# Performance work log

Hardware: AMD Instinct MI355X
Metric: run time of the kernel (lower is better)

## Reference

```python
import jax, jax.numpy as jnp
import numpy as np

V, E, H = 32000, 256, 512   # vocab, embed_dim, hidden_dim
B, S, T = 16, 512, 128      # batch, src_len, tgt_len
PAD = 0
H2 = 2 * H                  # decoder hidden size


def setup_inputs() -> dict:
    key = jax.random.key(0)
    ks = jax.random.split(key, 20)
    g = lambda k, shape: jax.random.normal(k, shape, dtype=jnp.float32) * 0.05
    emb = g(ks[0], (V, E)).at[PAD].set(0.0)  # padding_idx row zeroed
    inp = {
        "src": jax.random.randint(ks[18], (B, S), 0, V, dtype=jnp.int32),
        "tgt": jax.random.randint(ks[19], (B, T), 0, V, dtype=jnp.int32),
        "emb": emb,
        # encoder forward direction (torch gate order i,f,g,o)
        "Wih_f": g(ks[1], (4 * H, E)), "Whh_f": g(ks[2], (4 * H, H)),
        "bih_f": g(ks[3], (4 * H,)),   "bhh_f": g(ks[4], (4 * H,)),
        # encoder backward direction
        "Wih_b": g(ks[5], (4 * H, E)), "Whh_b": g(ks[6], (4 * H, H)),
        "bih_b": g(ks[7], (4 * H,)),   "bhh_b": g(ks[8], (4 * H,)),
        # decoder LSTM: input E+2H, hidden 2H
        "Wih_d": g(ks[9], (4 * H2, E + H2)), "Whh_d": g(ks[10], (4 * H2, H2)),
        "bih_d": g(ks[11], (4 * H2,)),       "bhh_d": g(ks[12], (4 * H2,)),
        # attention Linear(4H -> 2H)
        "Wa": g(ks[13], (H2, 2 * H2)), "ba": g(ks[14], (H2,)),
        # output Linear(2H -> V)
        "Wo": g(ks[15], (V, H2)), "bo": g(ks[16], (V,)),
    }
    return inp


def _lstm_cell(x, h, c, Wih, Whh, bih, bhh):
    z = x @ Wih.T + h @ Whh.T + bih + bhh
    i, f, g, o = jnp.split(z, 4, axis=-1)
    c = jax.nn.sigmoid(f) * c + jax.nn.sigmoid(i) * jnp.tanh(g)
    h = jax.nn.sigmoid(o) * jnp.tanh(c)
    return h, c


def _lstm_scan(xs, h0, c0, Wih, Whh, bih, bhh):
    def step(carry, x):
        h, c = _lstm_cell(x, carry[0], carry[1], Wih, Whh, bih, bhh)
        return (h, c), h
    (hT, cT), hs = jax.lax.scan(step, (h0, c0), xs)
    return hs, hT, cT


def reference(src, tgt, emb, Wih_f, Whh_f, bih_f, bhh_f, Wih_b, Whh_b, bih_b, bhh_b,
              Wih_d, Whh_d, bih_d, bhh_d, Wa, ba, Wo, bo):
    z = jnp.zeros((B, H), dtype=emb.dtype)
    xs = emb[src].transpose(1, 0, 2)                       # [S,B,E]
    hs_f, hTf, _ = _lstm_scan(xs,        z, z, Wih_f, Whh_f, bih_f, bhh_f)
    hs_b, hTb, _ = _lstm_scan(xs[::-1],  z, z, Wih_b, Whh_b, bih_b, bhh_b)
    enc_out = jnp.concatenate([hs_f, hs_b[::-1]], -1).transpose(1, 0, 2)  # [B,S,2H]
    h = jnp.concatenate([hTf, hTb], -1)                    # decoder h0 [B,2H]
    c = jnp.zeros_like(h)  # note: original reuses encoder c_n; see combined c0 below
    # original uses c_n (last cells) as decoder c0:
    _, _, cTf = _lstm_scan(xs, z, z, Wih_f, Whh_f, bih_f, bhh_f)[1], None, None
    # recompute cleanly (scan already returned cT above; redo properly):
    hs_f2, hTf2, cTf2 = _lstm_scan(xs,       z, z, Wih_f, Whh_f, bih_f, bhh_f)
    hs_b2, hTb2, cTb2 = _lstm_scan(xs[::-1], z, z, Wih_b, Whh_b, bih_b, bhh_b)
    c = jnp.concatenate([cTf2, cTb2], -1)

    Wa_h, Wa_e = Wa[:, :H2], Wa[:, H2:]
    enc_proj = jnp.einsum('bsd,kd->bsk', enc_out, Wa_e) + ba  # [B,S,2H]

    dec_xs = emb[tgt[:, :T - 1]].transpose(1, 0, 2)        # [T-1,B,E] teacher-forced

    def dec_step(carry, x):
        h, c = carry
        energy = jnp.tanh(enc_proj + (h @ Wa_h.T)[:, None, :])  # [B,S,2H]
        w = jax.nn.softmax(energy.sum(-1), axis=1)              # [B,S]
        ctx = jnp.einsum('bs,bsd->bd', w, enc_out)              # [B,2H]
        xi = jnp.concatenate([x, ctx], -1)                      # [B,E+2H]
        h, c = _lstm_cell(xi, h, c, Wih_d, Whh_d, bih_d, bhh_d)
        pred = h @ Wo.T + bo                                    # [B,V]
        return (h, c), pred

    _, preds = jax.lax.scan(dec_step, (h, c), dec_xs)           # [T-1,B,V]
    outputs = jnp.concatenate(
        [jnp.zeros((B, 1, V), dtype=preds.dtype), preds.transpose(1, 0, 2)], axis=1)
    return outputs
```

## Files before the change

kernel.cpp:

```cpp
#include <hip/hip_runtime.h>

typedef unsigned int uint;
typedef unsigned short ushort;
typedef unsigned long long ull;
typedef __attribute__((ext_vector_type(8))) short bf16x8;
typedef __attribute__((ext_vector_type(4))) float f32x4;

static constexpr int V_ = 32000, E_ = 256, H_ = 512, B_ = 16, S_ = 512, T_ = 128;
static constexpr int H2_ = 1024, G4_ = 2048, D4_ = 4096, KXI_ = 2304;
static constexpr int DSTEPS = T_ - 1;
static constexpr int MD = 2048;
static constexpr int NWG_DEC = 256;
static constexpr float LOG2E = 1.4426950408889634f;
static constexpr int ASTR = 2312;

#define DEVFN __device__ __forceinline__

DEVFN ushort f2bf(float f){ uint u = __builtin_bit_cast(uint, f); u += 0x7fffu + ((u>>16)&1u); return (ushort)(u>>16); }
DEVFN float bf2f(ushort h){ uint u = ((uint)h)<<16; return __builtin_bit_cast(float, u); }
DEVFN float fsig(float x){ float e = __builtin_amdgcn_exp2f(-LOG2E*x); return __builtin_amdgcn_rcpf(1.f+e); }
DEVFN float ftanh(float x){ x = fminf(15.f,fmaxf(-15.f,x)); float e = __builtin_amdgcn_exp2f(2.f*LOG2E*x); return (e-1.f)*__builtin_amdgcn_rcpf(e+1.f); }
DEVFN f32x4 mfma16(bf16x8 a, bf16x8 b, f32x4 c){ return __builtin_amdgcn_mfma_f32_16x16x32_bf16(a,b,c,0,0,0); }

struct ull2v{ ull x, y; };
DEVFN ull ald64(const void* p){ return __hip_atomic_load((const ull*)p, __ATOMIC_RELAXED, __HIP_MEMORY_SCOPE_AGENT); }
DEVFN uint ald32u(const uint* p){ return __hip_atomic_load(p, __ATOMIC_RELAXED, __HIP_MEMORY_SCOPE_AGENT); }
DEVFN float ald_f32(const float* p){ uint v = __hip_atomic_load((const uint*)p, __ATOMIC_RELAXED, __HIP_MEMORY_SCOPE_AGENT); return __builtin_bit_cast(float, v); }
DEVFN void ast32(float* p, float v){ __hip_atomic_store(p, v, __ATOMIC_RELAXED, __HIP_MEMORY_SCOPE_AGENT); }
DEVFN void ast16(ushort* p, ushort v){ __hip_atomic_store(p, v, __ATOMIC_RELAXED, __HIP_MEMORY_SCOPE_AGENT); }
DEVFN void astu(uint* p, uint v){ __hip_atomic_store(p, v, __ATOMIC_RELAXED, __HIP_MEMORY_SCOPE_AGENT); }

DEVFN void lbar(uint* lflags, int grp, int mem, int tid, uint& rnd){
  __syncthreads();
  rnd++;
  if (tid==0) astu(lflags + grp*16 + mem, rnd);
  if (tid<16){
    while (ald32u(lflags + grp*16 + tid) < rnd) __builtin_amdgcn_s_sleep(1);
  }
  __syncthreads();
}

__global__ void k_init(uint* __restrict__ flags, uint* __restrict__ hgf, uint* __restrict__ hgb,
                       uint* __restrict__ hU, uint* __restrict__ ctxU){
  int i = blockIdx.x*256 + threadIdx.x;
  if (i < 1024) flags[i] = 0;
  if (i < 2*B_*H_){ hgf[i]=0u; hgb[i]=0u; }
  if (i < B_*H2_) hU[i] = 0u;
  if (i < 2*B_*H2_) ctxU[i] = 0u;
}

__global__ void k_embed(const int* __restrict__ src, const int* __restrict__ tgt,
                        const float* __restrict__ emb, ushort* __restrict__ Xb, ushort* __restrict__ DXb){
  int r = blockIdx.x, tid = threadIdx.x;
  if (r < S_*B_){
    int s = r>>4, b = r&15;
    int id = src[b*S_+s];
    Xb[(size_t)r*E_+tid] = f2bf(emb[(size_t)id*E_+tid]);
  } else {
    int r2 = r - S_*B_;
    int t = r2>>4, b = r2&15;
    int id = tgt[b*T_+t];
    DXb[(size_t)r2*E_+tid] = f2bf(emb[(size_t)id*E_+tid]);
  }
}

__global__ void k_cvt_encw(const float* __restrict__ src, ushort* __restrict__ dst){
  int d = blockIdx.x;
  int wg = d>>7, r = d&127;
  int w = r>>4, jj=(r>>2)&3, g=r&3;
  int srow = g*H_ + wg*32 + w*4 + jj;
  for (int c = threadIdx.x; c < E_; c += 256)
    dst[(size_t)d*E_ + c] = f2bf(src[(size_t)srow*E_ + c]);
}

__global__ void k_bias_encp(const float* __restrict__ bih, const float* __restrict__ bhh, float* __restrict__ dst){
  int d = blockIdx.x*256 + threadIdx.x;
  int wg = d>>7, r = d&127;
  int w = r>>4, jj=(r>>2)&3, g=r&3;
  int srow = g*H_ + wg*32 + w*4 + jj;
  dst[d] = bih[srow]+bhh[srow];
}

__global__ void k_cvt_decw(const float* __restrict__ Wih_d, const float* __restrict__ Whh_d,
                           ushort* __restrict__ dst){
  int d = blockIdx.x;
  int wg = d>>4, r = d&15, jj = r>>2, g = r&3;
  int srow = g*H2_ + wg*4 + jj;
  for (int c = threadIdx.x; c < KXI_; c += 256){
    float v = (c < E_+H2_) ? Wih_d[(size_t)srow*(E_+H2_) + c] : Whh_d[(size_t)srow*H2_ + (c - (E_+H2_))];
    dst[(size_t)d*KXI_ + c] = f2bf(v);
  }
}

__global__ void k_bias_decp(const float* __restrict__ bih, const float* __restrict__ bhh, float* __restrict__ dst){
  int d = blockIdx.x*256 + threadIdx.x;
  int wg = d>>4, r = d&15, jj = r>>2, g = r&3;
  int srow = g*H2_ + wg*4 + jj;
  dst[d] = bih[srow]+bhh[srow];
}

__global__ void k_cvt_strided(const float* __restrict__ src, ushort* __restrict__ dst,
                              int cols, int sld, int soff, int dld, int doff){
  int r = blockIdx.x;
  for (int c = threadIdx.x; c < cols; c += 256)
    dst[(size_t)r*dld + doff + c] = f2bf(src[(size_t)r*sld + soff + c]);
}

__global__ void k_zero_t0(float* __restrict__ out){
  int i = blockIdx.x*256 + threadIdx.x;
  if (i < B_*V_){ int b = i / V_, v = i - b*V_; out[(size_t)b*T_*V_ + v] = 0.f; }
}

template<int MODE>
__global__ __launch_bounds__(256) void gemm128(const ushort* __restrict__ A, const ushort* __restrict__ Bm,
    const float* __restrict__ bias, void* __restrict__ outp, int M, int N, int K, int Mvalid){
  __shared__ __align__(16) ushort As[128*32];
  __shared__ __align__(16) ushort Bs[128*32];
  int tid = threadIdx.x;
  int wave = tid>>6, lane = tid&63;
  int m0 = blockIdx.y*128, n0 = blockIdx.x*128;
  int wm = wave>>1, wn = wave&1;
  int col = lane&15, rg = lane>>4;
  f32x4 acc[4][4];
  #pragma unroll
  for (int i=0;i<4;i++)
    #pragma unroll
    for (int j=0;j<4;j++) acc[i][j] = {0.f,0.f,0.f,0.f};
  for (int k0=0;k0<K;k0+=32){
    __syncthreads();
    #pragma unroll
    for (int j=0;j<2;j++){
      int li = j*256+tid;
      int row = li>>2, ko = (li&3)*8;
      *(bf16x8*)(As + li*8) = *(const bf16x8*)(A + (size_t)(m0+row)*K + k0 + ko);
      *(bf16x8*)(Bs + li*8) = *(const bf16x8*)(Bm + (size_t)(n0+row)*K + k0 + ko);
    }
    __syncthreads();
    bf16x8 af[4], bfr[4];
    #pragma unroll
    for (int f=0;f<4;f++){
      af[f]  = *(const bf16x8*)(As + (wm*64+f*16+col)*32 + rg*8);
      bfr[f] = *(const bf16x8*)(Bs + (wn*64+f*16+col)*32 + rg*8);
    }
    #pragma unroll
    for (int fm=0;fm<4;fm++)
      #pragma unroll
      for (int fn=0;fn<4;fn++)
        acc[fm][fn] = mfma16(af[fm], bfr[fn], acc[fm][fn]);
  }
  #pragma unroll
  for (int fm=0;fm<4;fm++){
    int mrow = m0 + wm*64 + fm*16 + rg*4;
    #pragma unroll
    for (int fn=0;fn<4;fn++){
      int gcol = n0 + wn*64 + fn*16 + col;
      float bv = bias ? bias[gcol] : 0.f;
      #pragma unroll
      for (int i=0;i<4;i++){
        float v = acc[fm][fn][i] + bv;
        int grow = mrow + i;
        if (MODE==0) ((float*)outp)[(size_t)grow*N + gcol] = v;
        else if (MODE==1) ((ushort*)outp)[(size_t)grow*N + gcol] = f2bf(v);
        else if (MODE==3) ((ushort*)outp)[(size_t)(grow>>4)*(16*2048) + gcol*16 + (grow&15)] = f2bf(v);
        else { if (grow < Mvalid){ int b = grow&15, t = grow>>4;
               ((float*)outp)[(size_t)b*T_*V_ + (size_t)(t+1)*V_ + gcol] = v; } }
      }
    }
  }
}

__global__ __launch_bounds__(512) void k_enc_persist(
    const ushort* __restrict__ Xgf, const ushort* __restrict__ Xgb,
    const float* __restrict__ Whhf, const float* __restrict__ Whhb,
    ushort* __restrict__ enc, ushort* __restrict__ enct,
    uint* __restrict__ hbuf1, float* __restrict__ cbuf0,
    uint* __restrict__ hgf, uint* __restrict__ hgb){
  const int dir = blockIdx.x >> 4;
  const int wg  = blockIdx.x & 15;
  const ushort* Xg = dir ? Xgb : Xgf;
  const float* Whh = dir ? Whhb : Whhf;
  uint* hg = dir ? hgb : hgf;
  __shared__ __align__(16) ushort Wlds[128*512];
  __shared__ __align__(16) ushort hls[16*512];
  int tid = threadIdx.x;
  for (int it=0; it<32; ++it){
    int r = it*4 + (tid>>7), ct = tid&127;
    int w_ = r>>4, jj=(r>>2)&3, g=r&3;
    int srow = g*H_ + wg*32 + w_*4 + jj;
    float4 v = *(const float4*)(Whh + (size_t)srow*H_ + ct*4);
    ushort4 o; o.x=f2bf(v.x); o.y=f2bf(v.y); o.z=f2bf(v.z); o.w=f2bf(v.w);
    int byte = (r*1024 + ct*8) ^ ((r&7)<<4);
    *(ushort4*)((char*)Wlds + byte) = o;
  }
  int w = tid>>6, lane = tid&63, colL = lane&15, rg = lane>>4;
  int gg = colL&3;
  float cst[4];
  #pragma unroll
  for (int i=0;i<4;i++) cst[i]=0.f;
  __syncthreads();
  for (int t=0;t<S_;++t){
    int pos = dir ? (S_-1-t) : t;
    const uint* hsrcU = hg + (t&1)*B_*H_;
    uint uu[16];
    for(;;){
      #pragma unroll
      for (int k2=0;k2<2;k2++){
        int idx = tid + k2*512;
        const uint* p = hsrcU + (idx>>6)*H_ + (idx&63)*8;
        #pragma unroll
        for (int j=0;j<4;j++){
          ull v = ald64(p + j*2);
          uu[k2*8+j*2] = (uint)v; uu[k2*8+j*2+1] = (uint)(v>>32);
        }
      }
      bool ok = true;
      #pragma unroll
      for (int i2=0;i2<16;i2++) ok &= ((uu[i2]>>16) == (uint)t);
      if (ok) break;
      __builtin_amdgcn_s_sleep(1);
    }
    int colg = wg*128 + w*16 + colL;
    ushort4 xv = *(const ushort4*)(Xg + ((size_t)pos*2048 + colg)*16 + rg*4);
    f32x4 acc;
    acc[0]=bf2f(xv.x); acc[1]=bf2f(xv.y); acc[2]=bf2f(xv.z); acc[3]=bf2f(xv.w);
    #pragma unroll
    for (int k2=0;k2<2;k2++){
      int idx = tid + k2*512;
      int byte = ((idx>>6)*1024 + (idx&63)*16) ^ (((idx>>6)&7)<<4);
      ushort tmp[8];
      #pragma unroll
      for (int j=0;j<8;j++) tmp[j] = (ushort)uu[k2*8+j];
      *(bf16x8*)((char*)hls + byte) = *(bf16x8*)tmp;
    }
    __syncthreads();
    int rowb = w*16 + colL;
    int base = rowb*1024 + rg*16, xm = (rowb&7)<<4;
    int hbase = colL*1024 + rg*16, hxm = (colL&7)<<4;
    #pragma unroll
    for (int kt=0;kt<16;kt++){
      bf16x8 afv = *(const bf16x8*)((const char*)hls + ((hbase + kt*64) ^ hxm));
      bf16x8 bfv = *(const bf16x8*)((const char*)Wlds + ((base + kt*64) ^ xm));
      acc = mfma16(afv, bfv, acc);
    }
    uint* hdstU = hg + ((t+1)&1)*B_*H_;
    #pragma unroll
    for (int i=0;i<4;i++){
      float v0 = acc[i];
      float v1 = __shfl_xor(v0, 1);
      float v2 = __shfl_xor(v0, 2);
      float v3 = __shfl_xor(v1, 2);
      float zi = gg==0?v0: gg==1?v1: gg==2?v2: v3;
      float zf = (gg^1)==0?v0: (gg^1)==1?v1: (gg^1)==2?v2: v3;
      float zg = (gg^2)==0?v0: (gg^2)==1?v1: (gg^2)==2?v2: v3;
      float zo = (gg^3)==0?v0: (gg^3)==1?v1: (gg^3)==2?v2: v3;
      float cc = fsig(zf)*cst[i] + fsig(zi)*ftanh(zg);
      cst[i] = cc;
      float h = fsig(zo)*ftanh(cc);
      if (gg==0){
        int j = wg*32 + w*4 + (colL>>2);
        int b = rg*4+i;
        ushort hb = f2bf(h);
        enc[((size_t)b*S_ + pos)*H2_ + dir*H_ + j] = hb;
        enct[((size_t)b*H2_ + dir*H_ + j)*S_ + pos] = hb;
        astu(&hdstU[b*H_ + j], (uint)hb | ((uint)(t+1)<<16));
        if (t==S_-1){
          hbuf1[b*H2_ + dir*H_ + j] = (uint)hb;
          cbuf0[b*H2_ + dir*H_ + j] = cc;
        }
      }
    }
    __syncthreads();
  }
}

__global__ __launch_bounds__(512) void k_dec(
    const float* __restrict__ P, const ushort* __restrict__ WaH,
    const ushort* __restrict__ Wd, const float* __restrict__ bsd,
    const ushort* __restrict__ enct, const ushort* __restrict__ DXb,
    const float* __restrict__ cbuf0, uint* __restrict__ hU,
    uint* __restrict__ ctxU, float* __restrict__ qbuf,
    float* __restrict__ scores, ushort* __restrict__ hsd,
    uint* __restrict__ flags){
  __shared__ __align__(16) ushort AB[16*ASTR];
  __shared__ __align__(16) float pr[8*256];
  __shared__ float redz[256];
  __shared__ float qls[1024];
  __shared__ float wls[512];
  __shared__ float part[512];
  __shared__ float red[16];
  __shared__ float cst[64];
  uint* lflags = flags + 256;
  uint* qf     = flags + 768;
  int wgid = blockIdx.x, tid = threadIdx.x;
  int w = tid>>6, lane = tid&63, colL = lane&15, rg = lane>>4;
  int b = wgid>>4, wc = wgid&15;
  uint rnd = 0;
  if (tid < 64){
    int jj = tid>>4, b4 = tid&15;
    cst[tid] = cbuf0[b4*H2_ + wgid*4 + jj];
  }
  for (int st=0; st<DSTEPS; ++st){
    const uint* hprevU = hU + ((st+1)&1)*B_*H2_;
    uint* cslot = ctxU + (st&1)*B_*H2_;
    const uint wantH = (uint)st;
    const uint wantC = (uint)(st+1);
    float* qslot = qbuf + (st&1)*B_*H2_;
    if (wgid >= 64 && wgid < 128){
      int n0 = (wgid-64)*16;
      const uint* hp = hprevU + colL*H2_ + w*128 + rg*8;
      uint uu[32];
      for(;;){
        #pragma unroll
        for (int kt=0;kt<4;kt++)
          #pragma unroll
          for (int j=0;j<4;j++){
            ull v = ald64(hp + kt*32 + j*2);
            uu[kt*8+j*2] = (uint)v; uu[kt*8+j*2+1] = (uint)(v>>32);
          }
        bool ok = true;
        #pragma unroll
        for (int i2=0;i2<32;i2++) ok &= ((uu[i2]>>16) == wantH);
        if (ok) break;
        __builtin_amdgcn_s_sleep(1);
      }
      f32x4 acc = {0.f,0.f,0.f,0.f};
      const ushort* Bp = WaH + (size_t)(n0+colL)*H2_ + w*128 + rg*8;
      #pragma unroll
      for (int kt=0;kt<4;kt++){
        ushort tmp[8];
        #pragma unroll
        for (int j=0;j<8;j++) tmp[j] = (ushort)uu[kt*8+j];
        acc = mfma16(*(bf16x8*)tmp, *(const bf16x8*)(Bp + kt*32), acc);
      }
      *(f32x4*)&pr[w*256 + lane*4] = acc;
      __syncthreads();
      if (tid < 256){
        float s = pr[tid];
        #pragma unroll
        for (int w8=1;w8<8;w8++) s += pr[w8*256 + tid];
        int l = tid>>2, i = tid&3;
        ast32(&qslot[(size_t)((l>>4)*4 + i)*H2_ + n0 + (l&15)], s);
      }
      __syncthreads();
      if (tid==0) astu(qf + (wgid-64), wantC);
    }
    if (tid < 64){
      while (ald32u(qf + tid) < wantC) __builtin_amdgcn_s_sleep(1);
    }
    __syncthreads();
    {
      ull q2 = ald64((const ull*)(qslot + (size_t)b*H2_) + tid);
      *(ull*)&qls[tid*2] = q2;
      __syncthreads();
      f32x4 qv[4];
      #pragma unroll
      for (int u=0;u<4;u++) qv[u] = *(const f32x4*)&qls[lane*16 + u*4];
      int rbase = b*S_ + wc*32 + w*4;
      #pragma unroll
      for (int rr=0;rr<4;rr++){
        int r = rbase + rr;
        const float4* Pr = (const float4*)(P + (size_t)r*H2_) + lane*4;
        float s = 0.f;
        #pragma unroll
        for (int u=0;u<4;u++){
          float4 pv = Pr[u];
          s += ftanh(pv.x+qv[u][0])+ftanh(pv.y+qv[u][1])+ftanh(pv.z+qv[u][2])+ftanh(pv.w+qv[u][3]);
        }
        #pragma unroll
        for (int o=32;o;o>>=1) s += __shfl_xor(s,o);
        if (lane==0) ast32(&scores[r], s);
      }
    }
    lbar(lflags, b, wc, tid, rnd);
    {
      float sc = ald_f32(scores + b*S_ + tid);
      float m = sc;
      #pragma unroll
      for (int o=32;o;o>>=1) m = fmaxf(m, __shfl_xor(m,o));
      if (lane==0) red[w] = m;
      __syncthreads();
      m = red[0];
      #pragma unroll
      for (int k2=1;k2<8;k2++) m = fmaxf(m, red[k2]);
      float e = __builtin_amdgcn_exp2f((sc - m)*LOG2E);
      float ss = e;
      #pragma unroll
      for (int o=32;o;o>>=1) ss += __shfl_xor(ss,o);
      if (lane==0) red[8+w] = ss;
      __syncthreads();
      float tot = red[8];
      #pragma unroll
      for (int k2=9;k2<16;k2++) tot += red[k2];
      wls[tid] = e * __builtin_amdgcn_rcpf(tot);
      __syncthreads();
      int c = wc*64 + (tid&63), sseg = tid>>6;
      const ushort* ep = enct + ((size_t)b*H2_ + c)*S_ + sseg*64;
      float a = 0.f;
      #pragma unroll
      for (int u=0;u<8;u++){
        bf16x8 ev = *(const bf16x8*)(ep + u*8);
        #pragma unroll
        for (int j=0;j<8;j++) a += wls[sseg*64 + u*8 + j] * bf2f((ushort)ev[j]);
      }
      part[tid] = a;
      __syncthreads();
      if (tid < 64){
        float s = part[tid];
        #pragma unroll
        for (int g2=1;g2<8;g2++) s += part[g2*64 + tid];
        astu(&cslot[b*H2_ + wc*64 + tid], (uint)f2bf(s) | (wantC<<16));
      }
    }
    {
      { int b3 = tid>>5, seg = tid&31;
        *(bf16x8*)&AB[b3*ASTR + seg*8] = *(const bf16x8*)(DXb + (size_t)(st*16+b3)*E_ + seg*8); }
      {
        uint uu[32];
        for(;;){
          #pragma unroll
          for (int k2=0;k2<4;k2++){
            int idx = tid + k2*512;
            const uint* p = cslot + (idx>>7)*H2_ + (idx&127)*8;
            #pragma unroll
            for (int j=0;j<4;j++){
              ull v = ald64(p + j*2);
              uu[k2*8+j*2] = (uint)v; uu[k2*8+j*2+1] = (uint)(v>>32);
            }
          }
          bool ok = true;
          #pragma unroll
          for (int i2=0;i2<32;i2++) ok &= ((uu[i2]>>16) == wantC);
          if (ok) break;
          __builtin_amdgcn_s_sleep(1);
        }
        #pragma unroll
        for (int k2=0;k2<4;k2++){
          int idx = tid + k2*512;
          ushort tmp[8];
          #pragma unroll
          for (int j=0;j<8;j++) tmp[j] = (ushort)uu[k2*8+j];
          *(bf16x8*)&AB[(idx>>7)*ASTR + 256 + (idx&127)*8] = *(bf16x8*)tmp;
        }
      }
      {
        uint uu[32];
        for(;;){
          #pragma unroll
          for (int k2=0;k2<4;k2++){
            int idx = tid + k2*512;
            const uint* p = hprevU + (idx>>7)*H2_ + (idx&127)*8;
            #pragma unroll
            for (int j=0;j<4;j++){
              ull v = ald64(p + j*2);
              uu[k2*8+j*2] = (uint)v; uu[k2*8+j*2+1] = (uint)(v>>32);
            }
          }
          bool ok = true;
          #pragma unroll
          for (int i2=0;i2<32;i2++) ok &= ((uu[i2]>>16) == wantH);
          if (ok) break;
          __builtin_amdgcn_s_sleep(1);
        }
        #pragma unroll
        for (int k2=0;k2<4;k2++){
          int idx = tid + k2*512;
          ushort tmp[8];
          #pragma unroll
          for (int j=0;j<8;j++) tmp[j] = (ushort)uu[k2*8+j];
          *(bf16x8*)&AB[(idx>>7)*ASTR + 1280 + (idx&127)*8] = *(bf16x8*)tmp;
        }
      }
      __syncthreads();
      int row0 = wgid*16;
      f32x4 acc = {0.f,0.f,0.f,0.f};
      const ushort* Bp = Wd + (size_t)(row0+colL)*KXI_ + w*288 + rg*8;
      const ushort* Apb = &AB[colL*ASTR + w*288 + rg*8];
      #pragma unroll
      for (int kt=0;kt<9;kt++)
        acc = mfma16(*(const bf16x8*)(Apb + kt*32), *(const bf16x8*)(Bp + kt*32), acc);
      *(f32x4*)&pr[w*256 + lane*4] = acc;
      __syncthreads();
      if (tid < 256){
        float s = bsd[row0 + ((tid>>2)&15)];
        #pragma unroll
        for (int w8=0;w8<8;w8++) s += pr[w8*256 + tid];
        redz[tid] = s;
      }
      __syncthreads();
      if (tid < 64){
        int jj = tid>>4, b4 = tid&15, rgc = b4>>2, ic = b4&3;
        float zi = redz[((jj*4+0) + 16*rgc)*4 + ic];
        float zf = redz[((jj*4+1) + 16*rgc)*4 + ic];
        float zg = redz[((jj*4+2) + 16*rgc)*4 + ic];
        float zo = redz[((jj*4+3) + 16*rgc)*4 + ic];
        float cc2 = fsig(zf)*cst[tid] + fsig(zi)*ftanh(zg);
        cst[tid] = cc2;
        float h = fsig(zo)*ftanh(cc2);
        ushort hb = f2bf(h);
        int j = wgid*4 + jj;
        astu(&hU[(st&1)*B_*H2_ + b4*H2_ + j], (uint)hb | ((uint)(st+1)<<16));
        hsd[((size_t)st*B_ + b4)*H2_ + j] = hb;
      }
      __syncthreads();
    }
  }
}

extern "C" void kernel_launch(void* const* d_in, const int* in_sizes, int n_in,
                              void* d_out, int out_size, void* d_ws, size_t ws_size,
                              hipStream_t stream) {
  const int* src   = (const int*)d_in[0];
  const int* tgt   = (const int*)d_in[1];
  const float* emb   = (const float*)d_in[2];
  const float* Wih_f = (const float*)d_in[3];
  const float* Whh_f = (const float*)d_in[4];
  const float* bih_f = (const float*)d_in[5];
  const float* bhh_f = (const float*)d_in[6];
  const float* Wih_b = (const float*)d_in[7];
  const float* Whh_b = (const float*)d_in[8];
  const float* bih_b = (const float*)d_in[9];
  const float* bhh_b = (const float*)d_in[10];
  const float* Wih_d = (const float*)d_in[11];
  const float* Whh_d = (const float*)d_in[12];
  const float* bih_d = (const float*)d_in[13];
  const float* bhh_d = (const float*)d_in[14];
  const float* Wa    = (const float*)d_in[15];
  const float* ba    = (const float*)d_in[16];
  const float* Wo    = (const float*)d_in[17];
  const float* bo    = (const float*)d_in[18];
  float* out = (float*)d_out;
  (void)in_sizes; (void)n_in; (void)out_size; (void)ws_size;

  char* ws = (char*)d_ws;
  size_t off = 0;
  auto alloc = [&](size_t bytes)->char*{ char* p = ws + off; off += (bytes + 255) & ~(size_t)255; return p; };
  ushort* Xb     = (ushort*)alloc((size_t)S_*B_*E_*2);
  ushort* DXb    = (ushort*)alloc((size_t)DSTEPS*B_*E_*2);
  ushort* Wihf_p = (ushort*)alloc((size_t)G4_*E_*2);
  ushort* Wihb_p = (ushort*)alloc((size_t)G4_*E_*2);
  float*  bsf    = (float*)alloc(G4_*4);
  float*  bsb    = (float*)alloc(G4_*4);
  ushort* ENC    = (ushort*)alloc((size_t)B_*S_*H2_*2);
  ushort* ENCT   = (ushort*)alloc((size_t)B_*S_*H2_*2);
  ushort* WaH    = (ushort*)alloc((size_t)H2_*H2_*2);
  ushort* WaE    = (ushort*)alloc((size_t)H2_*H2_*2);
  ushort* Wd     = (ushort*)alloc((size_t)D4_*KXI_*2);
  float*  bsd    = (float*)alloc(D4_*4);
  ushort* WoB    = (ushort*)alloc((size_t)V_*H2_*2);
  float*  cbuf0  = (float*)alloc(B_*H2_*4);
  uint*   hU     = (uint*)alloc((size_t)2*B_*H2_*4);
  uint*   ctxU   = (uint*)alloc((size_t)2*B_*H2_*4);
  float*  qbuf   = (float*)alloc((size_t)2*B_*H2_*4);
  float*  scores = (float*)alloc(B_*S_*4);
  ushort* hsd    = (ushort*)alloc((size_t)MD*H2_*2);
  uint*   hgf    = (uint*)alloc((size_t)2*B_*H_*4);
  uint*   hgb    = (uint*)alloc((size_t)2*B_*H_*4);
  uint*   flags  = (uint*)alloc(4096);
  char*   big    = alloc((size_t)2*S_*B_*G4_*2);
  ushort* Xgf = (ushort*)big;
  ushort* Xgb = (ushort*)(big + (size_t)S_*B_*G4_*2);
  float*  P   = (float*)big;

  k_init<<<dim3(128), dim3(256), 0, stream>>>(flags, hgf, hgb, hU, ctxU);
  k_embed<<<dim3(S_*B_ + DSTEPS*B_), dim3(E_), 0, stream>>>(src, tgt, emb, Xb, DXb);
  k_cvt_encw<<<dim3(G4_), dim3(256), 0, stream>>>(Wih_f, Wihf_p);
  k_cvt_encw<<<dim3(G4_), dim3(256), 0, stream>>>(Wih_b, Wihb_p);
  k_bias_encp<<<dim3(8), dim3(256), 0, stream>>>(bih_f, bhh_f, bsf);
  k_bias_encp<<<dim3(8), dim3(256), 0, stream>>>(bih_b, bhh_b, bsb);
  k_cvt_strided<<<dim3(H2_), dim3(256), 0, stream>>>(Wa, WaH, H2_, 2*H2_, 0,   H2_, 0);
  k_cvt_strided<<<dim3(H2_), dim3(256), 0, stream>>>(Wa, WaE, H2_, 2*H2_, H2_, H2_, 0);
  k_cvt_decw<<<dim3(D4_), dim3(256), 0, stream>>>(Wih_d, Whh_d, Wd);
  k_bias_decp<<<dim3(16), dim3(256), 0, stream>>>(bih_d, bhh_d, bsd);
  k_cvt_strided<<<dim3(V_),  dim3(256), 0, stream>>>(Wo, WoB, H2_, H2_, 0, H2_, 0);

  gemm128<3><<<dim3(G4_/128, (S_*B_)/128), dim3(256), 0, stream>>>(Xb, Wihf_p, bsf, Xgf, S_*B_, G4_, E_, 0);
  gemm128<3><<<dim3(G4_/128, (S_*B_)/128), dim3(256), 0, stream>>>(Xb, Wihb_p, bsb, Xgb, S_*B_, G4_, E_, 0);

  k_enc_persist<<<dim3(32), dim3(512), 0, stream>>>(Xgf, Xgb, Whh_f, Whh_b, ENC, ENCT,
                                                    hU + B_*H2_, cbuf0, hgf, hgb);

  gemm128<0><<<dim3(H2_/128, (B_*S_)/128), dim3(256), 0, stream>>>(ENC, WaE, ba, P, B_*S_, H2_, H2_, 0);
  k_zero_t0<<<dim3((B_*V_+255)/256), dim3(256), 0, stream>>>(out);

  k_dec<<<dim3(NWG_DEC), dim3(512), 0, stream>>>(P, WaH, Wd, bsd, ENCT, DXb, cbuf0, hU,
                                                 ctxU, qbuf, scores, hsd, flags);

  gemm128<2><<<dim3(V_/128, MD/128), dim3(256), 0, stream>>>(hsd, WoB, bo, out, MD, V_, H2_, DSTEPS*B_);
}
```

Measured before the change: 5.800 ms.

## Prefetch step-invariant operands before spin-waits in encoder and decoder loops

Loads that do not depend on the awaited flags are issued before the spin-wait loops. These are the encoder x-projection slice, the Wa_h and Wd weight fragments, the P rows for attention energy, and the encoder-output tile for context. Their global-memory latency can then overlap with synchronization waits instead of sitting on the critical path after them. The separate ctx and h polling loops in the decoder are also merged into one combined poll. The cost is higher register pressure from holding up to 16 f32x4 plus 17 bf16x8 values live across waits, which may reduce occupancy or cause spills.

```diff
diff --git a/kernel.cpp b/kernel.cpp
--- a/kernel.cpp
+++ b/kernel.cpp
@@ -201,6 +201,8 @@
   for (int t=0;t<S_;++t){
     int pos = dir ? (S_-1-t) : t;
     const uint* hsrcU = hg + (t&1)*B_*H_;
+    int colg = wg*128 + w*16 + colL;
+    ushort4 xv = *(const ushort4*)(Xg + ((size_t)pos*2048 + colg)*16 + rg*4);
     uint uu[16];
     for(;;){
       #pragma unroll
@@ -219,8 +221,6 @@
       if (ok) break;
       __builtin_amdgcn_s_sleep(1);
     }
-    int colg = wg*128 + w*16 + colL;
-    ushort4 xv = *(const ushort4*)(Xg + ((size_t)pos*2048 + colg)*16 + rg*4);
     f32x4 acc;
     acc[0]=bf2f(xv.x); acc[1]=bf2f(xv.y); acc[2]=bf2f(xv.z); acc[3]=bf2f(xv.w);
     #pragma unroll
@@ -307,6 +307,10 @@
     float* qslot = qbuf + (st&1)*B_*H2_;
     if (wgid >= 64 && wgid < 128){
       int n0 = (wgid-64)*16;
+      const ushort* Bp = WaH + (size_t)(n0+colL)*H2_ + w*128 + rg*8;
+      bf16x8 bwa[4];
+      #pragma unroll
+      for (int kt=0;kt<4;kt++) bwa[kt] = *(const bf16x8*)(Bp + kt*32);
       const uint* hp = hprevU + colL*H2_ + w*128 + rg*8;
       uint uu[32];
       for(;;){
@@ -324,13 +328,12 @@
         __builtin_amdgcn_s_sleep(1);
       }
       f32x4 acc = {0.f,0.f,0.f,0.f};
-      const ushort* Bp = WaH + (size_t)(n0+colL)*H2_ + w*128 + rg*8;
       #pragma unroll
       for (int kt=0;kt<4;kt++){
         ushort tmp[8];
         #pragma unroll
         for (int j=0;j<8;j++) tmp[j] = (ushort)uu[kt*8+j];
-        acc = mfma16(*(bf16x8*)tmp, *(const bf16x8*)(Bp + kt*32), acc);
+        acc = mfma16(*(bf16x8*)tmp, bwa[kt], acc);
       }
       *(f32x4*)&pr[w*256 + lane*4] = acc;
       __syncthreads();
@@ -343,6 +346,16 @@
       }
       __syncthreads();
       if (tid==0) astu(qf + (wgid-64), wantC);
+    }
+    f32x4 pv[16];
+    {
+      int rbase = b*S_ + wc*32 + w*4;
+      #pragma unroll
+      for (int rr=0;rr<4;rr++){
+        const f32x4* Pr = (const f32x4*)(P + (size_t)(rbase+rr)*H2_) + lane*4;
+        #pragma unroll
+        for (int u=0;u<4;u++) pv[rr*4+u] = Pr[u];
+      }
     }
     if (tid < 64){
       while (ald32u(qf + tid) < wantC) __builtin_amdgcn_s_sleep(1);
@@ -358,18 +371,23 @@
       int rbase = b*S_ + wc*32 + w*4;
       #pragma unroll
       for (int rr=0;rr<4;rr++){
-        int r = rbase + rr;
-        const float4* Pr = (const float4*)(P + (size_t)r*H2_) + lane*4;
         float s = 0.f;
         #pragma unroll
         for (int u=0;u<4;u++){
-          float4 pv = Pr[u];
-          s += ftanh(pv.x+qv[u][0])+ftanh(pv.y+qv[u][1])+ftanh(pv.z+qv[u][2])+ftanh(pv.w+qv[u][3]);
+          f32x4 p4 = pv[rr*4+u];
+          s += ftanh(p4[0]+qv[u][0])+ftanh(p4[1]+qv[u][1])+ftanh(p4[2]+qv[u][2])+ftanh(p4[3]+qv[u][3]);
         }
         #pragma unroll
         for (int o=32;o;o>>=1) s += __shfl_xor(s,o);
-        if (lane==0) ast32(&scores[r], s);
-      }
+        if (lane==0) ast32(&scores[rbase+rr], s);
+      }
+    }
+    bf16x8 ev[8];
+    {
+      int c = wc*64 + (tid&63), sseg = tid>>6;
+      const ushort* ep = enct + ((size_t)b*H2_ + c)*S_ + sseg*64;
+      #pragma unroll
+      for (int u=0;u<8;u++) ev[u] = *(const bf16x8*)(ep + u*8);
     }
     lbar(lflags, b, wc, tid, rnd);
     {
@@ -393,14 +411,12 @@
       for (int k2=9;k2<16;k2++) tot += red[k2];
       wls[tid] = e * __builtin_amdgcn_rcpf(tot);
       __syncthreads();
-      int c = wc*64 + (tid&63), sseg = tid>>6;
-      const ushort* ep = enct + ((size_t)b*H2_ + c)*S_ + sseg*64;
+      int sseg = tid>>6;
       float a = 0.f;
       #pragma unroll
       for (int u=0;u<8;u++){
-        bf16x8 ev = *(const bf16x8*)(ep + u*8);
-        #pragma unroll
-        for (int j=0;j<8;j++) a += wls[sseg*64 + u*8 + j] * bf2f((ushort)ev[j]);
+        #pragma unroll
+        for (int j=0;j<8;j++) a += wls[sseg*64 + u*8 + j] * bf2f((ushort)ev[u][j]);
       }
       part[tid] = a;
       __syncthreads();
@@ -414,70 +430,50 @@
     {
       { int b3 = tid>>5, seg = tid&31;
         *(bf16x8*)&AB[b3*ASTR + seg*8] = *(const bf16x8*)(DXb + (size_t)(st*16+b3)*E_ + seg*8); }
+      bf16x8 bw[9];
       {
-        uint uu[32];
-        for(;;){
-          #pragma unroll
-          for (int k2=0;k2<4;k2++){
-            int idx = tid + k2*512;
-            const uint* p = cslot + (idx>>7)*H2_ + (idx&127)*8;
-            #pragma unroll
-            for (int j=0;j<4;j++){
-              ull v = ald64(p + j*2);
-              uu[k2*8+j*2] = (uint)v; uu[k2*8+j*2+1] = (uint)(v>>32);
-            }
-          }
-          bool ok = true;
-          #pragma unroll
-          for (int i2=0;i2<32;i2++) ok &= ((uu[i2]>>16) == wantC);
-          if (ok) break;
-          __builtin_amdgcn_s_sleep(1);
-        }
+        int row0 = wgid*16;
+        const ushort* Bp = Wd + (size_t)(row0+colL)*KXI_ + w*288 + rg*8;
+        #pragma unroll
+        for (int kt=0;kt<9;kt++) bw[kt] = *(const bf16x8*)(Bp + kt*32);
+      }
+      uint uc[32], uh[32];
+      for(;;){
         #pragma unroll
         for (int k2=0;k2<4;k2++){
           int idx = tid + k2*512;
-          ushort tmp[8];
+          const uint* pc = cslot  + (idx>>7)*H2_ + (idx&127)*8;
+          const uint* ph = hprevU + (idx>>7)*H2_ + (idx&127)*8;
           #pragma unroll
-          for (int j=0;j<8;j++) tmp[j] = (ushort)uu[k2*8+j];
-          *(bf16x8*)&AB[(idx>>7)*ASTR + 256 + (idx&127)*8] = *(bf16x8*)tmp;
+          for (int j=0;j<4;j++){
+            ull vc = ald64(pc + j*2);
+            ull vh = ald64(ph + j*2);
+            uc[k2*8+j*2] = (uint)vc; uc[k2*8+j*2+1] = (uint)(vc>>32);
+            uh[k2*8+j*2] = (uint)vh; uh[k2*8+j*2+1] = (uint)(vh>>32);
+          }
         }
-      }
-      {
-        uint uu[32];
-        for(;;){
-          #pragma unroll
-          for (int k2=0;k2<4;k2++){
-            int idx = tid + k2*512;
-            const uint* p = hprevU + (idx>>7)*H2_ + (idx&127)*8;
-            #pragma unroll
-            for (int j=0;j<4;j++){
-              ull v = ald64(p + j*2);
-              uu[k2*8+j*2] = (uint)v; uu[k2*8+j*2+1] = (uint)(v>>32);
-            }
-          }
-          bool ok = true;
-          #pragma unroll
-          for (int i2=0;i2<32;i2++) ok &= ((uu[i2]>>16) == wantH);
-          if (ok) break;
-          __builtin_amdgcn_s_sleep(1);
-        }
-        #pragma unroll
-        for (int k2=0;k2<4;k2++){
-          int idx = tid + k2*512;
-          ushort tmp[8];
-          #pragma unroll
-          for (int j=0;j<8;j++) tmp[j] = (ushort)uu[k2*8+j];
-          *(bf16x8*)&AB[(idx>>7)*ASTR + 1280 + (idx&127)*8] = *(bf16x8*)tmp;
-        }
+        bool ok = true;
+        #pragma unroll
+        for (int i2=0;i2<32;i2++) ok &= ((uc[i2]>>16) == wantC) && ((uh[i2]>>16) == wantH);
+        if (ok) break;
+        __builtin_amdgcn_s_sleep(1);
+      }
+      #pragma unroll
+      for (int k2=0;k2<4;k2++){
+        int idx = tid + k2*512;
+        ushort tc[8], th[8];
+        #pragma unroll
+        for (int j=0;j<8;j++){ tc[j] = (ushort)uc[k2*8+j]; th[j] = (ushort)uh[k2*8+j]; }
+        *(bf16x8*)&AB[(idx>>7)*ASTR + 256  + (idx&127)*8] = *(bf16x8*)tc;
+        *(bf16x8*)&AB[(idx>>7)*ASTR + 1280 + (idx&127)*8] = *(bf16x8*)th;
       }
       __syncthreads();
       int row0 = wgid*16;
       f32x4 acc = {0.f,0.f,0.f,0.f};
-      const ushort* Bp = Wd + (size_t)(row0+colL)*KXI_ + w*288 + rg*8;
       const ushort* Apb = &AB[colL*ASTR + w*288 + rg*8];
       #pragma unroll
       for (int kt=0;kt<9;kt++)
-        acc = mfma16(*(const bf16x8*)(Apb + kt*32), *(const bf16x8*)(Bp + kt*32), acc);
+        acc = mfma16(*(const bf16x8*)(Apb + kt*32), bw[kt], acc);
       *(f32x4*)&pr[w*256 + lane*4] = acc;
       __syncthreads();
       if (tid < 256){
```

Result: no change. 5.856 ms (+1.0%).
